# Performance work log

Hardware: AMD Instinct MI355X
Metric: run time of the kernel (lower is better)

Reference implementation:

```python
import jax, jax.numpy as jnp
import numpy as np

B, NEG = 2, 16            # queries, negatives per query
N, E, D = 10000, 80000, 128  # nodes, edges, feature dim (in_dim == out_dim)
NUM_REL = 237
L = 3                     # PNA layers
NODE_RATIO = 0.1
K = max(1, int(NODE_RATIO * N))  # static top-k: every repeated graph has exactly N nodes
EPS = 1e-5


def _score(hidden, rel, lin_W, lin_b, m1_W, m1_b, m2_W, m2_b):
    heur = jnp.concatenate([hidden, rel], axis=-1) @ lin_W + lin_b
    x = heur * hidden
    h = jax.nn.relu(x @ m1_W + m1_b)
    return jnp.squeeze(h @ m2_W + m2_b, -1)


def _pna_conv(hidden, src, dst, emask, deg, pre_W, pre_b, post_W, post_b, out_W, out_b):
    """PNA layer with mean/max/min/std aggregators and identity/amplification/attenuation
    scalers, restricted to edges where emask is True. deg is the (clamped >=1) degree used
    by the scalers."""
    BN = hidden.shape[0]
    # message: pre-linear on [x_i (target), x_j (source)] per edge  -> (Erep, D)
    m = jnp.concatenate([hidden[dst], hidden[src]], axis=-1) @ pre_W + pre_b
    w = emask.astype(hidden.dtype)[:, None]
    cnt = jax.ops.segment_sum(emask.astype(hidden.dtype), dst, num_segments=BN)
    denom = jnp.maximum(cnt, 1.0)[:, None]
    s1 = jax.ops.segment_sum(m * w, dst, num_segments=BN)
    s2 = jax.ops.segment_sum(m * m * w, dst, num_segments=BN)
    mean = s1 / denom
    var = jax.nn.relu(s2 / denom - mean * mean)
    std = jnp.sqrt(var + EPS)
    has = (cnt > 0)[:, None]
    mx = jnp.where(has, jax.ops.segment_max(jnp.where(emask[:, None], m, -jnp.inf), dst, num_segments=BN), 0.0)
    mn = jnp.where(has, jax.ops.segment_min(jnp.where(emask[:, None], m, jnp.inf), dst, num_segments=BN), 0.0)
    agg = jnp.concatenate([mean, mx, mn, std], axis=-1)           # (BN, 4D)
    logd = jnp.log(deg + 1.0)                                     # deg >= 1 -> logd > 0
    avg_log = jnp.mean(logd)
    agg = jnp.concatenate([agg, agg * (logd / avg_log)[:, None], agg * (avg_log / logd)[:, None]], axis=-1)  # (BN, 12D)
    return (agg @ post_W + post_b) @ out_W + out_b


def _forward(h_index, r_index, t_index, hidden_states, edge_index, rel_embedding,
             lin_W, lin_b, m1_W, m1_b, m2_W, m2_b, pre_W, pre_b, post_W, post_b, out_W, out_b):
    sc = (lin_W, lin_b, m1_W, m1_b, m2_W, m2_b)
    # negative_sample_to_tail
    is_t_neg = jnp.all(h_index == h_index[:, :1], axis=-1, keepdims=True)
    h_idx = jnp.where(is_t_neg, h_index, t_index)
    t_idx = jnp.where(is_t_neg, t_index, h_index)
    r_idx = jnp.where(is_t_neg, r_index, r_index + NUM_REL)
    # repeat_graph
    offsets = jnp.arange(B, dtype=h_idx.dtype) * N               # (B,)
    src = jnp.tile(edge_index[0], B) + jnp.repeat(offsets, E)    # (B*E,)
    dst = jnp.tile(edge_index[1], B) + jnp.repeat(offsets, E)
    BN = B * N
    rel_embeds = rel_embedding[r_idx[:, 0]].astype(hidden_states.dtype)  # (B, D)
    flat_h = h_idx[:, 0] + offsets
    flat_t = t_idx[:, 0] + offsets
    # literal `repeat_interleave(N, dim=0)[:B]` quirk -> row arange(B)//N of gathered embs
    sel = jnp.arange(B) // N
    h_vals = hidden_states[h_idx[:, 0]][sel]                     # (B, D)
    t_vals = hidden_states[t_idx[:, 0]][sel]
    # init_input_embeds: boundary condition + initial score at head nodes
    boundary = jnp.zeros((BN, D), hidden_states.dtype).at[flat_t].set(t_vals).at[flat_h].set(h_vals)
    score = jnp.zeros(BN, jnp.float32).at[flat_h].set(_score(h_vals, rel_embeds, *sc))
    hidden = boundary
    rel_per_node = jnp.repeat(rel_embeds, N, axis=0)             # (BN, D), rel_embeds[batch_rep]
    rows = jnp.arange(B)[:, None]
    for l in range(L):
        # select_edges_pyg with degree_ratio=1.0: all out-edges of per-graph top-k nodes
        _, idx = jax.lax.top_k(score.reshape(B, N), K)           # (B, K)
        node_sel = jnp.zeros((B, N), bool).at[rows, idx].set(True).reshape(-1)
        emask = node_sel[src]                                    # (B*E,) selected-edge mask
        out_deg = jax.ops.segment_sum(emask.astype(jnp.float32), src, num_segments=BN)
        deg_sub = jnp.maximum(out_deg.astype(hidden.dtype), 1.0)
        new_hidden = _pna_conv(hidden, src, dst, emask, deg_sub,
                               pre_W[l], pre_b[l], post_W[l], post_b[l], out_W[l], out_b[l])
        # residual only for nodes with selected outgoing edges
        hidden = jnp.where((out_deg > 0)[:, None], hidden + new_hidden, hidden)
        score = _score(hidden, rel_per_node, *sc)
    # read out scores at (repeated) tail indices -> (B, NEG)
    return score[t_idx + offsets[:, None]]


def setup_inputs() -> dict:
    key = jax.random.key(0)
    ks = jax.random.split(key, 14)
    s = 0.05
    hi = jax.random.randint(ks[0], (B, 1), 0, N)
    h_index = jnp.tile(hi, (1, NEG))                 # constant per row (assert in forward)
    r0 = jax.random.randint(ks[1], (B, 1), 0, NUM_REL)
    r_index = jnp.tile(r0, (1, NEG))                 # constant per row (assert in forward)
    t_index = jax.random.randint(ks[2], (B, NEG), 0, N)
    hidden_states = jax.random.normal(ks[3], (N, D), jnp.float32)
    edge_index = jax.random.randint(ks[4], (2, E), 0, N)
    return {
        "h_index": h_index, "r_index": r_index, "t_index": t_index,
        "hidden_states": hidden_states, "edge_index": edge_index,
        "rel_embedding": jax.random.normal(ks[5], (2 * NUM_REL, D), jnp.float32) * s,
        "lin_W": jax.random.normal(ks[6], (2 * D, D), jnp.float32) * s, "lin_b": jnp.zeros(D, jnp.float32),
        "m1_W": jax.random.normal(ks[7], (D, D), jnp.float32) * s, "m1_b": jnp.zeros(D, jnp.float32),
        "m2_W": jax.random.normal(ks[8], (D, 1), jnp.float32) * s, "m2_b": jnp.zeros(1, jnp.float32),
        "pre_W": jax.random.normal(ks[9], (L, 2 * D, D), jnp.float32) * s, "pre_b": jnp.zeros((L, D), jnp.float32),
        "post_W": jax.random.normal(ks[10], (L, 12 * D, D), jnp.float32) * s, "post_b": jnp.zeros((L, D), jnp.float32),
        "out_W": jax.random.normal(ks[11], (L, D, D), jnp.float32) * s, "out_b": jnp.zeros((L, D), jnp.float32),
    }


def reference(h_index, r_index, t_index, hidden_states, edge_index, rel_embedding,
              lin_W, lin_b, m1_W, m1_b, m2_W, m2_b, pre_W, pre_b, post_W, post_b, out_W, out_b):
    return _forward(h_index, r_index, t_index, hidden_states, edge_index, rel_embedding,
                    lin_W, lin_b, m1_W, m1_b, m2_W, m2_b, pre_W, pre_b, post_W, post_b, out_W, out_b)
```

## Files before the change

kernel.cpp:

```cpp
#include <hip/hip_runtime.h>
#include <math.h>

#define Bq 2
#define NEG 16
#define Nn 10000
#define Ee 80000
#define Dd 128
#define NUM_REL 237
#define Ll 3
#define K_SEL 1000
#define BN (Bq*Nn)
#define EPSV 1e-5f
#define MAXACT 2048
#define MAXTOUCH 8192
#define SELCAP 3328
#define LN2F 0.69314718056f

constexpr size_t HID_OFF   = 0;
constexpr size_t SCORE_OFF = HID_OFF   + (size_t)BN*Dd*4;
constexpr size_t CVEC_OFF  = SCORE_OFF + (size_t)BN*4;
constexpr size_t HDR_OFF   = CVEC_OFF  + (size_t)Bq*Dd*4;
constexpr size_t THR_OFF   = HDR_OFF   + 64*4;
constexpr size_t SEL_OFF   = THR_OFF   + Bq*8;
constexpr size_t DEG_OFF   = SEL_OFF   + (size_t)BN*4;
constexpr size_t SLOT_OFF  = DEG_OFF   + (size_t)BN*4;
constexpr size_t CNT_OFF   = SLOT_OFF  + (size_t)BN*4;
constexpr size_t SDEG_OFF  = CNT_OFF   + (size_t)MAXACT*4;
constexpr size_t S1_OFF    = SDEG_OFF  + (size_t)MAXACT*4;
constexpr size_t S2_OFF    = S1_OFF    + (size_t)MAXACT*Dd*4;
constexpr size_t MXB_OFF   = S2_OFF    + (size_t)MAXACT*Dd*4;
constexpr size_t MNB_OFF   = MXB_OFF   + (size_t)MAXACT*Dd*4;
constexpr size_t TPART_OFF = MNB_OFF   + (size_t)MAXACT*Dd*4;
constexpr size_t ALIST_OFF = TPART_OFF + (size_t)4*MAXACT*Dd*4;
constexpr size_t FLAG_OFF  = ALIST_OFF + (size_t)MAXACT*4;
constexpr size_t TLIST_OFF = FLAG_OFF  + (size_t)BN*4;
constexpr size_t EDGE_OFF  = TLIST_OFF + (size_t)MAXTOUCH*4;
constexpr size_t CTR_OFF   = EDGE_OFF  + (size_t)Bq*Ee*2*4;

__device__ __forceinline__ unsigned encf(float f){
  unsigned u = __float_as_uint(f);
  return (u & 0x80000000u) ? ~u : (u | 0x80000000u);
}
__device__ __forceinline__ float decf(unsigned e){
  unsigned u = (e & 0x80000000u) ? (e & 0x7FFFFFFFu) : ~e;
  return __uint_as_float(u);
}
__device__ __forceinline__ unsigned long long make_key(float f, int i){
  unsigned d = ~encf(f);
  return ((unsigned long long)d << 32) | (unsigned)i;
}

__global__ void k_zero(float* hidden, unsigned* flag){
  int i = blockIdx.x*blockDim.x + threadIdx.x;
  if (i < BN*Dd/4) ((float4*)hidden)[i] = make_float4(0.f,0.f,0.f,0.f);
  if (i < BN) flag[i] = 0u;
}

__global__ __launch_bounds__(256) void k_prep(
    const int* h_index, const int* r_index, const int* t_index,
    const float* hidden_states, const float* rel_embedding,
    const float* lin_W, const float* lin_b, const float* m1_W, const float* m1_b,
    const float* m2_W, const float* m2_b,
    int* hdr, float* cvec, float* hidden, float* score,
    unsigned* flag, int* tlist, unsigned* ctr){
  __shared__ int sh_fh[Bq], sh_ft[Bq], sh_r0[Bq], sh_hsrc, sh_tsrc;
  __shared__ float s_relv[Bq][Dd], s_cvec[Bq][Dd], s_hv[Dd], s_x[Bq][Dd], s_p[Bq][Dd];
  __shared__ float s_s0[Dd];
  __shared__ float sc0_sh;
  int tid = threadIdx.x;
  if (tid == 0){
    int n = 0;
    for (int b=0;b<Bq;b++){
      bool eq = true;
      for (int j=1;j<NEG;j++) eq = eq && (h_index[b*NEG+j]==h_index[b*NEG]);
      int h0 = eq ? h_index[b*NEG] : t_index[b*NEG];
      int t0 = eq ? t_index[b*NEG] : h_index[b*NEG];
      int r0 = eq ? r_index[b*NEG] : r_index[b*NEG] + NUM_REL;
      sh_fh[b] = h0 + b*Nn; sh_ft[b] = t0 + b*Nn; sh_r0[b] = r0;
      hdr[0+b] = sh_fh[b]; hdr[2+b] = sh_ft[b];
      for (int j=0;j<NEG;j++){
        int tj = eq ? t_index[b*NEG+j] : h_index[b*NEG+j];
        hdr[4 + b*NEG + j] = tj + b*Nn;
      }
      if (b==0){ sh_hsrc = h0; sh_tsrc = t0; }
      if (!flag[sh_ft[b]]){ flag[sh_ft[b]] = 1u; tlist[n++] = sh_ft[b]; }
      if (!flag[sh_fh[b]]){ flag[sh_fh[b]] = 1u; tlist[n++] = sh_fh[b]; }
    }
    ctr[3] = (unsigned)n;
  }
  __syncthreads();
  int b = tid >> 7, d = tid & 127;
  s_relv[b][d] = rel_embedding[(size_t)sh_r0[b]*Dd + d];
  if (b == 0){
    s_hv[d] = hidden_states[(size_t)sh_hsrc*Dd + d];
    s_s0[d] = fmaxf(m1_b[d], 0.f) * m2_W[d];
  }
  __syncthreads();
  if (tid == 0){
    float s = m2_b[0];
    for (int k=0;k<Dd;k++) s += s_s0[k];
    sc0_sh = s;
    ctr[4] = __float_as_uint(s);
  }
  float acc = lin_b[d];
  #pragma unroll 8
  for (int k=0;k<Dd;k++) acc += s_relv[b][k]*lin_W[(Dd+k)*Dd + d];
  s_cvec[b][d] = acc; cvec[b*Dd+d] = acc;
  hidden[(size_t)sh_ft[b]*Dd + d] = hidden_states[(size_t)sh_tsrc*Dd + d];
  hidden[(size_t)sh_fh[b]*Dd + d] = hidden_states[(size_t)sh_hsrc*Dd + d];
  __syncthreads();
  float sc0 = sc0_sh;
  for (int i = tid; i < BN; i += 256) score[i] = sc0;
  float hv = s_hv[d];
  float heur = s_cvec[b][d];
  #pragma unroll 8
  for (int k=0;k<Dd;k++) heur += s_hv[k]*lin_W[k*Dd + d];
  s_x[b][d] = heur * hv;
  __syncthreads();
  float a2 = m1_b[d];
  #pragma unroll 8
  for (int k=0;k<Dd;k++) a2 += s_x[b][k]*m1_W[k*Dd + d];
  s_p[b][d] = fmaxf(a2, 0.f) * m2_W[d];
  __syncthreads();
  if (tid < Bq){
    float s = m2_b[0];
    for (int k=0;k<Dd;k++) s += s_p[tid][k];
    score[sh_fh[tid]] = s;
  }
}

__global__ __launch_bounds__(256) void k_select(
    const float* score, const int* tlist, const unsigned* ctr,
    unsigned long long* thr){
  int b = blockIdx.x;
  int nt = (int)ctr[3];
  unsigned d0 = ~encf(__uint_as_float(ctr[4]));
  __shared__ unsigned sd[SELCAP];
  __shared__ unsigned short sidx[SELCAP];
  __shared__ unsigned hist[256], histT[256];
  __shared__ int ntb_sh;
  __shared__ unsigned long long pref_sh;
  __shared__ unsigned kk_sh;
  int tid = threadIdx.x;
  if (tid==0){ ntb_sh = 0; pref_sh = 0ull; kk_sh = K_SEL; }
  __syncthreads();
  int vlo = b*Nn, vhi = vlo + Nn;
  for (int i = tid; i < nt; i += 256){
    int v = tlist[i];
    if (v >= vlo && v < vhi){
      int pos = atomicAdd(&ntb_sh, 1);
      if (pos < SELCAP){
        sd[pos] = ~encf(score[v]);
        sidx[pos] = (unsigned short)(v - vlo);
      }
    }
  }
  __syncthreads();
  int ntb = min(ntb_sh, SELCAP);
  unsigned nvirt = (unsigned)(Nn - ntb);
  for (int pass = 7; pass >= 0; --pass){
    hist[tid] = 0u; histT[tid] = 0u;
    __syncthreads();
    unsigned long long pref = pref_sh;
    int sh_hi = 8*(pass+1);
    for (int j = tid; j < ntb; j += 256){
      unsigned long long key = ((unsigned long long)sd[j] << 32) | (unsigned long long)sidx[j];
      bool ok = (pass==7) || ((key >> sh_hi) == (pref >> sh_hi));
      if (ok) atomicAdd(&hist[(unsigned)(key >> (8*pass)) & 255u], 1u);
      if (pass < 4){
        unsigned idx = sidx[j];
        bool oki = (pass == 3) || ((idx >> sh_hi) == (((unsigned)pref) >> sh_hi));
        if (oki) atomicAdd(&histT[(idx >> (8*pass)) & 255u], 1u);
      }
    }
    __syncthreads();
    if (pass >= 4){
      if (tid == 0){
        unsigned long long keyv_hi = ((unsigned long long)d0 << 32);
        bool ok = (pass==7) || ((keyv_hi >> sh_hi) == (pref >> sh_hi));
        if (ok) atomicAdd(&hist[(d0 >> (8*(pass-4))) & 255u], nvirt);
      }
    } else {
      if ((unsigned)(pref >> 32) == d0){
        unsigned long long hf = 0ull;
        if (pass < 3) hf = (unsigned long long)((((unsigned)pref) >> sh_hi)) << sh_hi;
        unsigned long long lo = hf + ((unsigned long long)tid << (8*pass));
        unsigned long long hi = lo + (1ull << (8*pass));
        unsigned long long nn = (unsigned long long)Nn;
        unsigned long long l2 = lo < nn ? lo : nn;
        unsigned long long h2 = hi < nn ? hi : nn;
        if (h2 > l2){
          unsigned c = (unsigned)(h2 - l2) - histT[tid];
          if (c > 0u) atomicAdd(&hist[tid], c);
        }
      }
    }
    __syncthreads();
    if (tid < 256){
      unsigned kk = kk_sh;
      unsigned cum = 0;
      for (int i=0;i<tid;i++) cum += hist[i];
      unsigned h = hist[tid];
      if (h > 0u && cum < kk && kk <= cum + h){
        pref_sh |= ((unsigned long long)tid) << (8*pass);
        kk_sh = kk - cum;
      }
    }
    __syncthreads();
  }
  if (tid==0) thr[b] = pref_sh;
}

__global__ void k_mask(const float* score, const unsigned long long* thr, unsigned* sel,
                       unsigned* out_deg, float* s1, float* s2,
                       unsigned* mxb, unsigned* mnb, unsigned* cnt, unsigned* ctr){
  int i = blockIdx.x*blockDim.x + threadIdx.x;
  if (i < BN){
    int b = i / Nn; int v = i - b*Nn;
    sel[i] = (make_key(score[i], v) <= thr[b]) ? 1u : 0u;
    out_deg[i] = 0u;
  }
  if (i < MAXACT*Dd){ s1[i]=0.f; s2[i]=0.f; mxb[i]=0u; mnb[i]=0xFFFFFFFFu; }
  if (i < MAXACT) cnt[i]=0u;
  if (i < 3) ctr[i]=0u;
}

__global__ void k_degree(const int* ei, const unsigned* sel, unsigned* out_deg){
  int e = blockIdx.x*blockDim.x + threadIdx.x;
  if (e >= Ee) return;
  int s0 = ei[e];
  #pragma unroll
  for (int b=0;b<Bq;b++){
    int v = s0 + b*Nn;
    if (sel[v]) atomicAdd(&out_deg[v], 1u);
  }
}

__global__ void k_active(const unsigned* out_deg, int* node_slot, int* alist,
                         float* slot_deg, unsigned* ctr, unsigned* flag, int* tlist){
  int v = blockIdx.x*blockDim.x + threadIdx.x;
  if (v >= BN) return;
  unsigned dg = out_deg[v];
  if (dg > 0u){
    int slot = (int)atomicAdd(&ctr[0], 1u);
    alist[slot] = v; node_slot[v] = slot; slot_deg[slot] = (float)dg;
    atomicAdd((float*)&ctr[2], logf((float)dg + 1.0f));
    if (atomicExch(&flag[v], 1u) == 0u){
      int p = (int)atomicAdd(&ctr[3], 1u);
      tlist[p] = v;
    }
  }
}

__global__ void k_edges(const int* ei, const unsigned* sel, const unsigned* out_deg,
                        const int* node_slot, int* edges, unsigned* cnt, unsigned* ctr){
  int e = blockIdx.x*blockDim.x + threadIdx.x;
  if (e >= Ee) return;
  int s0 = ei[e], d0 = ei[Ee + e];
  #pragma unroll
  for (int b=0;b<Bq;b++){
    int s = s0 + b*Nn, dv = d0 + b*Nn;
    if (sel[s] && out_deg[dv] > 0u){
      int slot = node_slot[dv];
      int j = (int)atomicAdd(&ctr[1], 1u);
      edges[2*j] = s; edges[2*j+1] = slot;
      atomicAdd(&cnt[slot], 1u);
    }
  }
}

__global__ __launch_bounds__(128) void k_messages(
    const float* hidden, const int* edges, const int* alist,
    const float* preW, const float* preb,
    float* s1, float* s2, unsigned* mxb, unsigned* mnb, const unsigned* ctr){
  int ne = (int)ctr[1];
  int tid = threadIdx.x;
  __shared__ float sd[4][Dd], ss[4][Dd];
  __shared__ int dsl[4];
  float pb = preb[tid];
  for (int j0 = blockIdx.x*4; j0 < ne; j0 += gridDim.x*4){
    int nv = ne - j0; if (nv > 4) nv = 4;
    if (tid < 4){
      int j = j0 + ((tid < nv) ? tid : 0);
      dsl[tid] = edges[2*j+1];
    }
    #pragma unroll
    for (int e=0;e<4;e++){
      int j = j0 + ((e < nv) ? e : 0);
      int s = edges[2*j];
      int dv = alist[edges[2*j+1]];
      sd[e][tid] = hidden[(size_t)dv*Dd + tid];
      ss[e][tid] = hidden[(size_t)s*Dd + tid];
    }
    __syncthreads();
    float a[4] = {pb, pb, pb, pb};
    #pragma unroll 4
    for (int k=0;k<Dd;k++){
      float w0 = preW[k*Dd + tid];
      float w1 = preW[(Dd+k)*Dd + tid];
      #pragma unroll
      for (int e=0;e<4;e++) a[e] += sd[e][k]*w0 + ss[e][k]*w1;
    }
    for (int e=0;e<nv;e++){
      int dslot = dsl[e];
      atomicAdd(&s1[dslot*Dd + tid], a[e]);
      atomicAdd(&s2[dslot*Dd + tid], a[e]*a[e]);
      atomicMax(&mxb[dslot*Dd + tid], encf(a[e]));
      atomicMin(&mnb[dslot*Dd + tid], encf(a[e]));
    }
    __syncthreads();
  }
}

__global__ __launch_bounds__(512) void k_post(
    const unsigned* cnt, const float* s1, const float* s2,
    const unsigned* mxb, const unsigned* mnb, const float* slot_deg,
    const float* postW, float* tpart, const unsigned* ctr){
  int na = (int)ctr[0];
  int bid = blockIdx.x;
  int tile = bid & 63, ch = bid >> 6;
  if (tile*32 >= na) return;
  float logsum = __uint_as_float(ctr[2]);
  float avg = (logsum + (float)(BN - na)*LN2F) / (float)BN;
  __shared__ float lb[32*136];
  __shared__ float wbuf[3*16*128];
  __shared__ float sden[32];
  __shared__ unsigned shas[32];
  int tid = threadIdx.x;
  if (tid < 32){
    unsigned c = cnt[tile*32 + tid];
    sden[tid] = fmaxf((float)c, 1.0f);
    shas[tid] = c;
  }
  __syncthreads();
  for (int idx = tid; idx < 32*Dd; idx += 512){
    int sl = idx >> 7, kk = idx & 127;
    int gi = (tile*32 + sl)*Dd + kk;
    float den = sden[sl];
    float val;
    if (ch == 0)      val = s1[gi]/den;
    else if (ch == 1) val = shas[sl] ? decf(mxb[gi]) : 0.f;
    else if (ch == 2) val = shas[sl] ? decf(mnb[gi]) : 0.f;
    else {
      float mv = s1[gi]/den;
      float var = s2[gi]/den - mv*mv;
      val = sqrtf(fmaxf(var, 0.f) + EPSV);
    }
    lb[sl*136 + kk] = val;
  }
  int cg = tid & 31, rg = tid >> 5;
  int c0 = cg*4;
  float a0[2][4], a1[2][4], a2[2][4];
  #pragma unroll
  for (int i=0;i<2;i++)
    #pragma unroll
    for (int j=0;j<4;j++){ a0[i][j]=0.f; a1[i][j]=0.f; a2[i][j]=0.f; }
  for (int chunk = 0; chunk < 8; ++chunk){
    #pragma unroll
    for (int i = 0; i < 3; ++i){
      int f = tid + i*512;
      int q = f >> 9, r = f & 511;
      int kk = r >> 5, c4 = r & 31;
      int grow = q*512 + ch*128 + chunk*16 + kk;
      ((float4*)wbuf)[f] = *(const float4*)(postW + (size_t)grow*Dd + c4*4);
    }
    __syncthreads();
    #pragma unroll
    for (int k4 = 0; k4 < 4; ++k4){
      float4 av0 = *(const float4*)&lb[(rg*2+0)*136 + chunk*16 + k4*4];
      float4 av1 = *(const float4*)&lb[(rg*2+1)*136 + chunk*16 + k4*4];
      #pragma unroll
      for (int j = 0; j < 4; ++j){
        int kk = k4*4 + j;
        float4 w0 = *(const float4*)&wbuf[kk*128 + c0];
        float4 w1 = *(const float4*)&wbuf[(16+kk)*128 + c0];
        float4 w2 = *(const float4*)&wbuf[(32+kk)*128 + c0];
        float av[2] = { (&av0.x)[j], (&av1.x)[j] };
        #pragma unroll
        for (int i=0;i<2;i++){
          float a = av[i];
          a0[i][0] += a*w0.x; a0[i][1] += a*w0.y; a0[i][2] += a*w0.z; a0[i][3] += a*w0.w;
          a1[i][0] += a*w1.x; a1[i][1] += a*w1.y; a1[i][2] += a*w1.z; a1[i][3] += a*w1.w;
          a2[i][0] += a*w2.x; a2[i][1] += a*w2.y; a2[i][2] += a*w2.z; a2[i][3] += a*w2.w;
        }
      }
    }
    __syncthreads();
  }
  #pragma unroll
  for (int i=0;i<2;i++){
    int slot = tile*32 + rg*2 + i;
    if (slot < na){
      float dg = slot_deg[slot];
      float logd = logf(dg + 1.f);
      float al = logd/avg, be = avg/logd;
      float4 r;
      r.x = a0[i][0] + al*a1[i][0] + be*a2[i][0];
      r.y = a0[i][1] + al*a1[i][1] + be*a2[i][1];
      r.z = a0[i][2] + al*a1[i][2] + be*a2[i][2];
      r.w = a0[i][3] + al*a1[i][3] + be*a2[i][3];
      *(float4*)(tpart + (size_t)ch*MAXACT*Dd + (size_t)slot*Dd + c0) = r;
    }
  }
}

__global__ __launch_bounds__(256) void k_out_resid(
    const float* tpart, const int* alist, const float* outW, const float* outb,
    const float* postb, float* hidden, const unsigned* ctr){
  int na = (int)ctr[0];
  int tile = blockIdx.x;
  if (tile*32 >= na) return;
  __shared__ float tr[32*136];
  __shared__ float wbuf[16*128];
  int tid = threadIdx.x;
  for (int idx = tid; idx < 32*Dd; idx += 256){
    int sl = idx >> 7, kk = idx & 127;
    size_t o = (size_t)(tile*32 + sl)*Dd + kk;
    tr[sl*136 + kk] = tpart[o] + tpart[(size_t)MAXACT*Dd + o]
                    + tpart[(size_t)2*MAXACT*Dd + o] + tpart[(size_t)3*MAXACT*Dd + o]
                    + postb[kk];
  }
  int cg = tid & 31, rg = tid >> 5;
  int c0 = cg*4;
  float4 ob = *(const float4*)(outb + c0);
  float acc[4][4];
  #pragma unroll
  for (int r=0;r<4;r++){ acc[r][0]=ob.x; acc[r][1]=ob.y; acc[r][2]=ob.z; acc[r][3]=ob.w; }
  for (int chunk = 0; chunk < 8; ++chunk){
    #pragma unroll
    for (int i = 0; i < 2; ++i){
      int f = tid + i*256;
      int kk = f >> 5, c4 = f & 31;
      ((float4*)wbuf)[f] = *(const float4*)(outW + (size_t)(chunk*16 + kk)*Dd + c4*4);
    }
    __syncthreads();
    #pragma unroll
    for (int k4 = 0; k4 < 4; ++k4){
      float4 av[4];
      #pragma unroll
      for (int r=0;r<4;r++)
        av[r] = *(const float4*)&tr[(rg*4+r)*136 + chunk*16 + k4*4];
      #pragma unroll
      for (int j = 0; j < 4; ++j){
        float4 w = *(const float4*)&wbuf[(k4*4+j)*128 + c0];
        #pragma unroll
        for (int r=0;r<4;r++){
          float a = (&av[r].x)[j];
          acc[r][0] += a*w.x; acc[r][1] += a*w.y; acc[r][2] += a*w.z; acc[r][3] += a*w.w;
        }
      }
    }
    __syncthreads();
  }
  #pragma unroll
  for (int r=0;r<4;r++){
    int slot = tile*32 + rg*4 + r;
    if (slot < na){
      int v = alist[slot];
      float* hp = hidden + (size_t)v*Dd + c0;
      float4 h4 = *(float4*)hp;
      h4.x += acc[r][0]; h4.y += acc[r][1]; h4.z += acc[r][2]; h4.w += acc[r][3];
      *(float4*)hp = h4;
    }
  }
}

__global__ __launch_bounds__(256) void k_score(
    const float* hidden, const float* cvec, const float* linW,
    const float* m1W, const float* m1b, const float* m2W, const float* m2b,
    const int* tlist, const unsigned* ctr, float* score,
    const int* ovr, int ovr_n){
  int nt = (ovr_n > 0) ? ovr_n : (int)ctr[3];
  const int* list = (ovr_n > 0) ? ovr : tlist;
  int nb = blockIdx.x * 32;
  if (nb >= nt) return;
  __shared__ float sh[32*Dd];
  __shared__ float sx[32*Dd];
  __shared__ float sc[2*Dd];
  __shared__ int   sv[32];
  __shared__ float red[32*33];
  int tid = threadIdx.x;
  if (tid < 32){
    int idx = nb + tid;
    sv[tid] = (idx < nt) ? list[idx] : list[nb];
  }
  sc[tid] = cvec[tid];
  __syncthreads();
  for (int q = tid; q < 32*32; q += 256){
    int row = q >> 5, f4 = q & 31;
    ((float4*)sh)[row*32 + f4] = ((const float4*)(hidden + (size_t)sv[row]*Dd))[f4];
  }
  __syncthreads();
  int cg = tid & 31, rg = tid >> 5;
  int c0 = cg*4;
  float acc[4][4];
  #pragma unroll
  for (int i=0;i<4;i++){ acc[i][0]=0.f; acc[i][1]=0.f; acc[i][2]=0.f; acc[i][3]=0.f; }
  for (int k4=0;k4<32;k4++){
    float4 av[4];
    #pragma unroll
    for (int i=0;i<4;i++) av[i] = ((float4*)sh)[(rg*4+i)*32 + k4];
    #pragma unroll
    for (int j=0;j<4;j++){
      float4 w = *(const float4*)(linW + (size_t)(k4*4+j)*Dd + c0);
      #pragma unroll
      for (int i=0;i<4;i++){
        float a = (&av[i].x)[j];
        acc[i][0] += a*w.x; acc[i][1] += a*w.y; acc[i][2] += a*w.z; acc[i][3] += a*w.w;
      }
    }
  }
  #pragma unroll
  for (int i=0;i<4;i++){
    int row = rg*4 + i;
    int bb = (sv[row] >= Nn) ? 1 : 0;
    float4 cv = *(float4*)&sc[bb*Dd + c0];
    float4 hv = ((float4*)sh)[row*32 + cg];
    float4 x;
    x.x = (acc[i][0] + cv.x)*hv.x;
    x.y = (acc[i][1] + cv.y)*hv.y;
    x.z = (acc[i][2] + cv.z)*hv.z;
    x.w = (acc[i][3] + cv.w)*hv.w;
    ((float4*)sx)[row*32 + cg] = x;
  }
  __syncthreads();
  #pragma unroll
  for (int i=0;i<4;i++){ acc[i][0]=0.f; acc[i][1]=0.f; acc[i][2]=0.f; acc[i][3]=0.f; }
  for (int k4=0;k4<32;k4++){
    float4 av[4];
    #pragma unroll
    for (int i=0;i<4;i++) av[i] = ((float4*)sx)[(rg*4+i)*32 + k4];
    #pragma unroll
    for (int j=0;j<4;j++){
      float4 w = *(const float4*)(m1W + (size_t)(k4*4+j)*Dd + c0);
      #pragma unroll
      for (int i=0;i<4;i++){
        float a = (&av[i].x)[j];
        acc[i][0] += a*w.x; acc[i][1] += a*w.y; acc[i][2] += a*w.z; acc[i][3] += a*w.w;
      }
    }
  }
  float4 mb = *(const float4*)(m1b + c0);
  float4 mw = *(const float4*)(m2W + c0);
  #pragma unroll
  for (int i=0;i<4;i++){
    float p0 = fmaxf(acc[i][0]+mb.x, 0.f)*mw.x;
    float p1 = fmaxf(acc[i][1]+mb.y, 0.f)*mw.y;
    float p2 = fmaxf(acc[i][2]+mb.z, 0.f)*mw.z;
    float p3 = fmaxf(acc[i][3]+mb.w, 0.f)*mw.w;
    red[(rg*4+i)*33 + cg] = p0+p1+p2+p3;
  }
  __syncthreads();
  if (tid < 32){
    float s = m2b[0];
    for (int g=0; g<32; g++) s += red[tid*33 + g];
    if (nb + tid < nt) score[sv[tid]] = s;
  }
}

__global__ void k_gather(const float* score, const int* hdr, float* out){
  int i = threadIdx.x;
  if (i < Bq*NEG) out[i] = score[hdr[4+i]];
}

extern "C" void kernel_launch(void* const* d_in, const int* in_sizes, int n_in,
                              void* d_out, int out_size, void* d_ws, size_t ws_size,
                              hipStream_t stream){
  const int*   h_index       = (const int*)d_in[0];
  const int*   r_index       = (const int*)d_in[1];
  const int*   t_index       = (const int*)d_in[2];
  const float* hidden_states = (const float*)d_in[3];
  const int*   edge_index    = (const int*)d_in[4];
  const float* rel_embedding = (const float*)d_in[5];
  const float* lin_W  = (const float*)d_in[6];
  const float* lin_b  = (const float*)d_in[7];
  const float* m1_W   = (const float*)d_in[8];
  const float* m1_b   = (const float*)d_in[9];
  const float* m2_W   = (const float*)d_in[10];
  const float* m2_b   = (const float*)d_in[11];
  const float* pre_W  = (const float*)d_in[12];
  const float* pre_b  = (const float*)d_in[13];
  const float* post_W = (const float*)d_in[14];
  const float* post_b = (const float*)d_in[15];
  const float* out_W  = (const float*)d_in[16];
  const float* out_b  = (const float*)d_in[17];

  char* ws = (char*)d_ws;
  float*    hidden   = (float*)(ws + HID_OFF);
  float*    score    = (float*)(ws + SCORE_OFF);
  float*    cvec     = (float*)(ws + CVEC_OFF);
  int*      hdr      = (int*)(ws + HDR_OFF);
  unsigned long long* thr = (unsigned long long*)(ws + THR_OFF);
  unsigned* sel      = (unsigned*)(ws + SEL_OFF);
  unsigned* out_deg  = (unsigned*)(ws + DEG_OFF);
  int*      node_slot= (int*)(ws + SLOT_OFF);
  unsigned* cnt      = (unsigned*)(ws + CNT_OFF);
  float*    slot_deg = (float*)(ws + SDEG_OFF);
  float*    s1       = (float*)(ws + S1_OFF);
  float*    s2       = (float*)(ws + S2_OFF);
  unsigned* mxb      = (unsigned*)(ws + MXB_OFF);
  unsigned* mnb      = (unsigned*)(ws + MNB_OFF);
  float*    tpart    = (float*)(ws + TPART_OFF);
  int*      alist    = (int*)(ws + ALIST_OFF);
  unsigned* flag     = (unsigned*)(ws + FLAG_OFF);
  int*      tlist    = (int*)(ws + TLIST_OFF);
  int*      edges    = (int*)(ws + EDGE_OFF);
  unsigned* ctr      = (unsigned*)(ws + CTR_OFF);

  k_zero<<<(BN*Dd/4 + 255)/256, 256, 0, stream>>>(hidden, flag);
  k_prep<<<1, 256, 0, stream>>>(h_index, r_index, t_index, hidden_states, rel_embedding,
                                lin_W, lin_b, m1_W, m1_b, m2_W, m2_b,
                                hdr, cvec, hidden, score, flag, tlist, ctr);
  for (int l = 0; l < Ll; ++l){
    const float* preWl  = pre_W  + (size_t)l*2*Dd*Dd;
    const float* prebl  = pre_b  + (size_t)l*Dd;
    const float* postWl = post_W + (size_t)l*12*Dd*Dd;
    const float* postbl = post_b + (size_t)l*Dd;
    const float* outWl  = out_W  + (size_t)l*Dd*Dd;
    const float* outbl  = out_b  + (size_t)l*Dd;

    k_select<<<Bq, 256, 0, stream>>>(score, tlist, ctr, thr);
    k_mask<<<(MAXACT*Dd + 255)/256, 256, 0, stream>>>(score, thr, sel, out_deg,
                                                      s1, s2, mxb, mnb, cnt, ctr);
    k_degree<<<(Ee + 255)/256, 256, 0, stream>>>(edge_index, sel, out_deg);
    k_active<<<(BN + 255)/256, 256, 0, stream>>>(out_deg, node_slot, alist, slot_deg,
                                                 ctr, flag, tlist);
    k_edges<<<(Ee + 255)/256, 256, 0, stream>>>(edge_index, sel, out_deg, node_slot,
                                                edges, cnt, ctr);
    k_messages<<<512, 128, 0, stream>>>(hidden, edges, alist, preWl, prebl,
                                        s1, s2, mxb, mnb, ctr);
    k_post<<<256, 512, 0, stream>>>(cnt, s1, s2, mxb, mnb, slot_deg, postWl, tpart, ctr);
    k_out_resid<<<MAXACT/32, 256, 0, stream>>>(tpart, alist, outWl, outbl, postbl,
                                               hidden, ctr);
    if (l < Ll-1){
      k_score<<<MAXTOUCH/32, 256, 0, stream>>>(hidden, cvec, lin_W, m1_W, m1_b, m2_W, m2_b,
                                               tlist, ctr, score, tlist, 0);
    } else {
      k_score<<<1, 256, 0, stream>>>(hidden, cvec, lin_W, m1_W, m1_b, m2_W, m2_b,
                                     tlist, ctr, score, hdr + 4, Bq*NEG);
    }
  }
  k_gather<<<1, 64, 0, stream>>>(score, hdr, (float*)d_out);
}
```

Measured before the change: 481.7 us.

## Fuse init, selection/zeroing and edge-build kernels to cut launches per layer

Merges the zeroing and prep kernels into one multi-block init kernel. The top-k select now shares a launch with the workspace zeroing, and the selection mask is computed inline from score and threshold instead of being stored in a sel array. The active-node and edge-list kernels are combined into one build kernel, the message kernel is relaunched with a different grid and indexed by node slot, and the final score kernel writes the output directly so the gather kernel is gone. The aim is to remove several small kernel launches and passes over global memory in each of the three layers, at the cost of more complex combined kernels and recomputing the mask keys inside each edge kernel.

```diff
diff --git a/kernel.cpp b/kernel.cpp
--- a/kernel.cpp
+++ b/kernel.cpp
@@ -21,8 +21,8 @@
 constexpr size_t CVEC_OFF  = SCORE_OFF + (size_t)BN*4;
 constexpr size_t HDR_OFF   = CVEC_OFF  + (size_t)Bq*Dd*4;
 constexpr size_t THR_OFF   = HDR_OFF   + 64*4;
-constexpr size_t SEL_OFF   = THR_OFF   + Bq*8;
-constexpr size_t DEG_OFF   = SEL_OFF   + (size_t)BN*4;
+constexpr size_t INC_OFF   = THR_OFF   + Bq*8;
+constexpr size_t DEG_OFF   = INC_OFF   + (size_t)BN*4;
 constexpr size_t SLOT_OFF  = DEG_OFF   + (size_t)BN*4;
 constexpr size_t CNT_OFF   = SLOT_OFF  + (size_t)BN*4;
 constexpr size_t SDEG_OFF  = CNT_OFF   + (size_t)MAXACT*4;
@@ -50,272 +50,312 @@
   return ((unsigned long long)d << 32) | (unsigned)i;
 }
 
-__global__ void k_zero(float* hidden, unsigned* flag){
-  int i = blockIdx.x*blockDim.x + threadIdx.x;
-  if (i < BN*Dd/4) ((float4*)hidden)[i] = make_float4(0.f,0.f,0.f,0.f);
-  if (i < BN) flag[i] = 0u;
-}
-
-__global__ __launch_bounds__(256) void k_prep(
-    const int* h_index, const int* r_index, const int* t_index,
-    const float* hidden_states, const float* rel_embedding,
-    const float* lin_W, const float* lin_b, const float* m1_W, const float* m1_b,
-    const float* m2_W, const float* m2_b,
-    int* hdr, float* cvec, float* hidden, float* score,
-    unsigned* flag, int* tlist, unsigned* ctr){
-  __shared__ int sh_fh[Bq], sh_ft[Bq], sh_r0[Bq], sh_hsrc, sh_tsrc;
-  __shared__ float s_relv[Bq][Dd], s_cvec[Bq][Dd], s_hv[Dd], s_x[Bq][Dd], s_p[Bq][Dd];
-  __shared__ float s_s0[Dd];
-  __shared__ float sc0_sh;
-  int tid = threadIdx.x;
-  if (tid == 0){
-    int n = 0;
-    for (int b=0;b<Bq;b++){
-      bool eq = true;
-      for (int j=1;j<NEG;j++) eq = eq && (h_index[b*NEG+j]==h_index[b*NEG]);
-      int h0 = eq ? h_index[b*NEG] : t_index[b*NEG];
-      int t0 = eq ? t_index[b*NEG] : h_index[b*NEG];
-      int r0 = eq ? r_index[b*NEG] : r_index[b*NEG] + NUM_REL;
-      sh_fh[b] = h0 + b*Nn; sh_ft[b] = t0 + b*Nn; sh_r0[b] = r0;
-      hdr[0+b] = sh_fh[b]; hdr[2+b] = sh_ft[b];
-      for (int j=0;j<NEG;j++){
-        int tj = eq ? t_index[b*NEG+j] : h_index[b*NEG+j];
-        hdr[4 + b*NEG + j] = tj + b*Nn;
-      }
-      if (b==0){ sh_hsrc = h0; sh_tsrc = t0; }
-      if (!flag[sh_ft[b]]){ flag[sh_ft[b]] = 1u; tlist[n++] = sh_ft[b]; }
-      if (!flag[sh_fh[b]]){ flag[sh_fh[b]] = 1u; tlist[n++] = sh_fh[b]; }
-    }
-    ctr[3] = (unsigned)n;
-  }
-  __syncthreads();
-  int b = tid >> 7, d = tid & 127;
-  s_relv[b][d] = rel_embedding[(size_t)sh_r0[b]*Dd + d];
-  if (b == 0){
-    s_hv[d] = hidden_states[(size_t)sh_hsrc*Dd + d];
-    s_s0[d] = fmaxf(m1_b[d], 0.f) * m2_W[d];
-  }
+__global__ __launch_bounds__(256) void k_init(
+    const int* __restrict__ h_index, const int* __restrict__ r_index, const int* __restrict__ t_index,
+    const float* __restrict__ hidden_states, const float* __restrict__ rel_embedding,
+    const float* __restrict__ lin_W, const float* __restrict__ lin_b,
+    const float* __restrict__ m1_W, const float* __restrict__ m1_b,
+    const float* __restrict__ m2_W, const float* __restrict__ m2_b,
+    int* __restrict__ hdr, float* __restrict__ cvec, float* __restrict__ hidden,
+    float* __restrict__ score, unsigned* __restrict__ flag, int* __restrict__ tlist,
+    unsigned* __restrict__ ctr)
+{
+  __shared__ struct {
+    int hbuf[Bq*NEG], tbuf[Bq*NEG], rbuf[Bq*NEG];
+    int fh[Bq], ft[Bq], r0[Bq], eqf[Bq], hsrc, tsrc;
+    float s0red[Dd]; float sc0;
+    float relv[Bq][Dd], cv[Bq][Dd], hv[Dd], x[Bq][Dd], p[Bq][Dd];
+  } sp;
+  const int tid = threadIdx.x;
+  const int bid = blockIdx.x;
+  if (tid < Bq*NEG){
+    sp.hbuf[tid] = h_index[tid];
+    sp.tbuf[tid] = t_index[tid];
+    sp.rbuf[tid] = r_index[tid];
+  }
+  if (tid < Dd) sp.s0red[tid] = fmaxf(m1_b[tid], 0.f) * m2_W[tid];
   __syncthreads();
   if (tid == 0){
+    for (int b = 0; b < Bq; b++){
+      bool eq = true;
+      for (int j = 1; j < NEG; j++) eq = eq && (sp.hbuf[b*NEG+j] == sp.hbuf[b*NEG]);
+      int h0 = eq ? sp.hbuf[b*NEG] : sp.tbuf[b*NEG];
+      int t0 = eq ? sp.tbuf[b*NEG] : sp.hbuf[b*NEG];
+      int r0 = eq ? sp.rbuf[b*NEG] : sp.rbuf[b*NEG] + NUM_REL;
+      sp.fh[b] = h0 + b*Nn; sp.ft[b] = t0 + b*Nn;
+      sp.r0[b] = r0; sp.eqf[b] = eq ? 1 : 0;
+      if (b == 0){ sp.hsrc = h0; sp.tsrc = t0; }
+    }
     float s = m2_b[0];
-    for (int k=0;k<Dd;k++) s += s_s0[k];
-    sc0_sh = s;
-    ctr[4] = __float_as_uint(s);
-  }
-  float acc = lin_b[d];
-  #pragma unroll 8
-  for (int k=0;k<Dd;k++) acc += s_relv[b][k]*lin_W[(Dd+k)*Dd + d];
-  s_cvec[b][d] = acc; cvec[b*Dd+d] = acc;
-  hidden[(size_t)sh_ft[b]*Dd + d] = hidden_states[(size_t)sh_tsrc*Dd + d];
-  hidden[(size_t)sh_fh[b]*Dd + d] = hidden_states[(size_t)sh_hsrc*Dd + d];
+    for (int k = 0; k < Dd; k++) s += sp.s0red[k];
+    sp.sc0 = s;
+    if (bid == 0){
+      ctr[4] = __float_as_uint(s);
+      hdr[0] = sp.fh[0]; hdr[1] = sp.fh[1];
+      hdr[2] = sp.ft[0]; hdr[3] = sp.ft[1];
+      for (int b = 0; b < Bq; b++)
+        for (int j = 0; j < NEG; j++){
+          int tj = sp.eqf[b] ? sp.tbuf[b*NEG+j] : sp.hbuf[b*NEG+j];
+          hdr[4 + b*NEG + j] = tj + b*Nn;
+        }
+      int cand[4] = { sp.ft[0], sp.fh[0], sp.ft[1], sp.fh[1] };
+      int n = 0;
+      for (int c = 0; c < 4; c++){
+        bool dup = false;
+        for (int m = 0; m < n; m++) dup = dup || (tlist[m] == cand[c]);
+        if (!dup) tlist[n++] = cand[c];
+        flag[cand[c]] = 1u;
+      }
+      ctr[3] = (unsigned)n;
+    }
+  }
   __syncthreads();
-  float sc0 = sc0_sh;
-  for (int i = tid; i < BN; i += 256) score[i] = sc0;
-  float hv = s_hv[d];
-  float heur = s_cvec[b][d];
-  #pragma unroll 8
-  for (int k=0;k<Dd;k++) heur += s_hv[k]*lin_W[k*Dd + d];
-  s_x[b][d] = heur * hv;
-  __syncthreads();
-  float a2 = m1_b[d];
-  #pragma unroll 8
-  for (int k=0;k<Dd;k++) a2 += s_x[b][k]*m1_W[k*Dd + d];
-  s_p[b][d] = fmaxf(a2, 0.f) * m2_W[d];
-  __syncthreads();
-  if (tid < Bq){
-    float s = m2_b[0];
-    for (int k=0;k<Dd;k++) s += s_p[tid][k];
-    score[sh_fh[tid]] = s;
-  }
-}
-
-__global__ __launch_bounds__(256) void k_select(
-    const float* score, const int* tlist, const unsigned* ctr,
-    unsigned long long* thr){
-  int b = blockIdx.x;
-  int nt = (int)ctr[3];
-  unsigned d0 = ~encf(__uint_as_float(ctr[4]));
-  __shared__ unsigned sd[SELCAP];
-  __shared__ unsigned short sidx[SELCAP];
-  __shared__ unsigned hist[256], histT[256];
-  __shared__ int ntb_sh;
-  __shared__ unsigned long long pref_sh;
-  __shared__ unsigned kk_sh;
+  const int fh0 = sp.fh[0], fh1 = sp.fh[1];
+  const int ft0 = sp.ft[0], ft1 = sp.ft[1];
+  const float sc0 = sp.sc0;
+  if (bid == 0){
+    int b = tid >> 7, d = tid & 127;
+    sp.relv[b][d] = rel_embedding[(size_t)sp.r0[b]*Dd + d];
+    if (b == 0) sp.hv[d] = hidden_states[(size_t)sp.hsrc*Dd + d];
+    __syncthreads();
+    float acc = lin_b[d];
+    #pragma unroll 8
+    for (int k = 0; k < Dd; k++) acc += sp.relv[b][k]*lin_W[(Dd+k)*Dd + d];
+    sp.cv[b][d] = acc; cvec[b*Dd + d] = acc;
+    hidden[(size_t)sp.ft[b]*Dd + d] = hidden_states[(size_t)sp.tsrc*Dd + d];
+    hidden[(size_t)sp.fh[b]*Dd + d] = hidden_states[(size_t)sp.hsrc*Dd + d];
+    __syncthreads();
+    float hv = sp.hv[d];
+    float heur = sp.cv[b][d];
+    #pragma unroll 8
+    for (int k = 0; k < Dd; k++) heur += sp.hv[k]*lin_W[k*Dd + d];
+    sp.x[b][d] = heur * hv;
+    __syncthreads();
+    float a2 = m1_b[d];
+    #pragma unroll 8
+    for (int k = 0; k < Dd; k++) a2 += sp.x[b][k]*m1_W[k*Dd + d];
+    sp.p[b][d] = fmaxf(a2, 0.f) * m2_W[d];
+    __syncthreads();
+    if (tid < Bq){
+      float s = m2_b[0];
+      for (int k = 0; k < Dd; k++) s += sp.p[tid][k];
+      score[sp.fh[tid]] = s;
+    }
+  } else {
+    int zb = bid - 1, znb = gridDim.x - 1;
+    int zt = zb*256 + tid, zs = znb*256;
+    float4 z4 = make_float4(0.f, 0.f, 0.f, 0.f);
+    for (int i = zt; i < BN*32; i += zs){
+      int row = i >> 5;
+      if (row != ft0 && row != ft1 && row != fh0 && row != fh1)
+        ((float4*)hidden)[i] = z4;
+    }
+    for (int v = zt; v < BN; v += zs){
+      if (v != ft0 && v != ft1 && v != fh0 && v != fh1) flag[v] = 0u;
+      if (v != fh0 && v != fh1) score[v] = sc0;
+    }
+  }
+}
+
+__global__ __launch_bounds__(256) void k_selzero(
+    const float* __restrict__ score, const int* __restrict__ tlist,
+    unsigned long long* __restrict__ thr,
+    float* __restrict__ s1, float* __restrict__ s2,
+    unsigned* __restrict__ mxb, unsigned* __restrict__ mnb,
+    unsigned* __restrict__ out_deg, unsigned* __restrict__ incnt,
+    unsigned* __restrict__ ctr)
+{
   int tid = threadIdx.x;
-  if (tid==0){ ntb_sh = 0; pref_sh = 0ull; kk_sh = K_SEL; }
-  __syncthreads();
-  int vlo = b*Nn, vhi = vlo + Nn;
-  for (int i = tid; i < nt; i += 256){
-    int v = tlist[i];
-    if (v >= vlo && v < vhi){
-      int pos = atomicAdd(&ntb_sh, 1);
-      if (pos < SELCAP){
-        sd[pos] = ~encf(score[v]);
-        sidx[pos] = (unsigned short)(v - vlo);
-      }
-    }
-  }
-  __syncthreads();
-  int ntb = min(ntb_sh, SELCAP);
-  unsigned nvirt = (unsigned)(Nn - ntb);
-  for (int pass = 7; pass >= 0; --pass){
-    hist[tid] = 0u; histT[tid] = 0u;
-    __syncthreads();
-    unsigned long long pref = pref_sh;
-    int sh_hi = 8*(pass+1);
-    for (int j = tid; j < ntb; j += 256){
-      unsigned long long key = ((unsigned long long)sd[j] << 32) | (unsigned long long)sidx[j];
-      bool ok = (pass==7) || ((key >> sh_hi) == (pref >> sh_hi));
-      if (ok) atomicAdd(&hist[(unsigned)(key >> (8*pass)) & 255u], 1u);
-      if (pass < 4){
-        unsigned idx = sidx[j];
-        bool oki = (pass == 3) || ((idx >> sh_hi) == (((unsigned)pref) >> sh_hi));
-        if (oki) atomicAdd(&histT[(idx >> (8*pass)) & 255u], 1u);
-      }
-    }
-    __syncthreads();
-    if (pass >= 4){
-      if (tid == 0){
-        unsigned long long keyv_hi = ((unsigned long long)d0 << 32);
-        bool ok = (pass==7) || ((keyv_hi >> sh_hi) == (pref >> sh_hi));
-        if (ok) atomicAdd(&hist[(d0 >> (8*(pass-4))) & 255u], nvirt);
-      }
-    } else {
-      if ((unsigned)(pref >> 32) == d0){
-        unsigned long long hf = 0ull;
-        if (pass < 3) hf = (unsigned long long)((((unsigned)pref) >> sh_hi)) << sh_hi;
-        unsigned long long lo = hf + ((unsigned long long)tid << (8*pass));
-        unsigned long long hi = lo + (1ull << (8*pass));
-        unsigned long long nn = (unsigned long long)Nn;
-        unsigned long long l2 = lo < nn ? lo : nn;
-        unsigned long long h2 = hi < nn ? hi : nn;
-        if (h2 > l2){
-          unsigned c = (unsigned)(h2 - l2) - histT[tid];
-          if (c > 0u) atomicAdd(&hist[tid], c);
-        }
-      }
-    }
-    __syncthreads();
-    if (tid < 256){
-      unsigned kk = kk_sh;
-      unsigned cum = 0;
-      for (int i=0;i<tid;i++) cum += hist[i];
-      unsigned h = hist[tid];
-      if (h > 0u && cum < kk && kk <= cum + h){
-        pref_sh |= ((unsigned long long)tid) << (8*pass);
-        kk_sh = kk - cum;
-      }
-    }
-    __syncthreads();
-  }
-  if (tid==0) thr[b] = pref_sh;
-}
-
-__global__ void k_mask(const float* score, const unsigned long long* thr, unsigned* sel,
-                       unsigned* out_deg, float* s1, float* s2,
-                       unsigned* mxb, unsigned* mnb, unsigned* cnt, unsigned* ctr){
+  int bid = blockIdx.x;
+  if (bid < Bq){
+    int b = bid;
+    int nt = (int)ctr[3];
+    unsigned d0 = ~encf(__uint_as_float(ctr[4]));
+    __shared__ unsigned sd[SELCAP];
+    __shared__ unsigned short sidx[SELCAP];
+    __shared__ unsigned hist[256], histT[256];
+    __shared__ int ntb_sh;
+    __shared__ unsigned long long pref_sh;
+    __shared__ unsigned kk_sh;
+    if (tid == 0){ ntb_sh = 0; pref_sh = 0ull; kk_sh = K_SEL; }
+    __syncthreads();
+    int vlo = b*Nn, vhi = vlo + Nn;
+    for (int i = tid; i < nt; i += 256){
+      int v = tlist[i];
+      if (v >= vlo && v < vhi){
+        int pos = atomicAdd(&ntb_sh, 1);
+        if (pos < SELCAP){
+          sd[pos] = ~encf(score[v]);
+          sidx[pos] = (unsigned short)(v - vlo);
+        }
+      }
+    }
+    __syncthreads();
+    int ntb = min(ntb_sh, SELCAP);
+    unsigned nvirt = (unsigned)(Nn - ntb);
+    for (int pass = 7; pass >= 0; --pass){
+      hist[tid] = 0u; histT[tid] = 0u;
+      __syncthreads();
+      unsigned long long pref = pref_sh;
+      int sh_hi = 8*(pass+1);
+      for (int j = tid; j < ntb; j += 256){
+        unsigned long long key = ((unsigned long long)sd[j] << 32) | (unsigned long long)sidx[j];
+        bool ok = (pass==7) || ((key >> sh_hi) == (pref >> sh_hi));
+        if (ok) atomicAdd(&hist[(unsigned)(key >> (8*pass)) & 255u], 1u);
+        if (pass < 4){
+          unsigned idx = sidx[j];
+          bool oki = (pass == 3) || ((idx >> sh_hi) == (((unsigned)pref) >> sh_hi));
+          if (oki) atomicAdd(&histT[(idx >> (8*pass)) & 255u], 1u);
+        }
+      }
+      __syncthreads();
+      if (pass >= 4){
+        if (tid == 0){
+          unsigned long long keyv_hi = ((unsigned long long)d0 << 32);
+          bool ok = (pass==7) || ((keyv_hi >> sh_hi) == (pref_sh >> sh_hi));
+          if (ok) atomicAdd(&hist[(d0 >> (8*(pass-4))) & 255u], nvirt);
+        }
+      } else {
+        if ((unsigned)(pref >> 32) == d0){
+          unsigned long long hf = 0ull;
+          if (pass < 3) hf = (unsigned long long)((((unsigned)pref) >> sh_hi)) << sh_hi;
+          unsigned long long lo = hf + ((unsigned long long)tid << (8*pass));
+          unsigned long long hi = lo + (1ull << (8*pass));
+          unsigned long long nn = (unsigned long long)Nn;
+          unsigned long long l2 = lo < nn ? lo : nn;
+          unsigned long long h2 = hi < nn ? hi : nn;
+          if (h2 > l2){
+            unsigned c = (unsigned)(h2 - l2) - histT[tid];
+            if (c > 0u) atomicAdd(&hist[tid], c);
+          }
+        }
+      }
+      __syncthreads();
+      {
+        unsigned kk = kk_sh;
+        unsigned cum = 0;
+        for (int i = 0; i < tid; i++) cum += hist[i];
+        unsigned h = hist[tid];
+        if (h > 0u && cum < kk && kk <= cum + h){
+          pref_sh |= ((unsigned long long)tid) << (8*pass);
+          kk_sh = kk - cum;
+        }
+      }
+      __syncthreads();
+    }
+    if (tid == 0) thr[b] = pref_sh;
+  } else {
+    int zb = bid - Bq, znb = gridDim.x - Bq;
+    int zt = zb*256 + tid, zs = znb*256;
+    for (int i = zt; i < MAXACT*Dd; i += zs){
+      s1[i] = 0.f; s2[i] = 0.f; mxb[i] = 0u; mnb[i] = 0xFFFFFFFFu;
+    }
+    for (int i = zt; i < BN; i += zs){ out_deg[i] = 0u; incnt[i] = 0u; }
+    if (zt < 3) ctr[zt] = 0u;
+  }
+}
+
+__global__ void k_degree(const int* __restrict__ ei, const float* __restrict__ score,
+                         const unsigned long long* __restrict__ thr,
+                         unsigned* __restrict__ out_deg){
+  int e = blockIdx.x*blockDim.x + threadIdx.x;
+  if (e >= Ee) return;
+  unsigned long long th0 = thr[0], th1 = thr[1];
+  int s0 = ei[e];
+  if (make_key(score[s0], s0) <= th0) atomicAdd(&out_deg[s0], 1u);
+  int v1 = s0 + Nn;
+  if (make_key(score[v1], s0) <= th1) atomicAdd(&out_deg[v1], 1u);
+}
+
+__global__ void k_build(const int* __restrict__ ei, const float* __restrict__ score,
+                        const unsigned long long* __restrict__ thr,
+                        const unsigned* __restrict__ out_deg,
+                        int* __restrict__ node_slot, int* __restrict__ alist,
+                        float* __restrict__ slot_deg, unsigned* __restrict__ incnt,
+                        int* __restrict__ edges, unsigned* __restrict__ ctr,
+                        unsigned* __restrict__ flag, int* __restrict__ tlist){
   int i = blockIdx.x*blockDim.x + threadIdx.x;
   if (i < BN){
-    int b = i / Nn; int v = i - b*Nn;
-    sel[i] = (make_key(score[i], v) <= thr[b]) ? 1u : 0u;
-    out_deg[i] = 0u;
-  }
-  if (i < MAXACT*Dd){ s1[i]=0.f; s2[i]=0.f; mxb[i]=0u; mnb[i]=0xFFFFFFFFu; }
-  if (i < MAXACT) cnt[i]=0u;
-  if (i < 3) ctr[i]=0u;
-}
-
-__global__ void k_degree(const int* ei, const unsigned* sel, unsigned* out_deg){
-  int e = blockIdx.x*blockDim.x + threadIdx.x;
-  if (e >= Ee) return;
-  int s0 = ei[e];
-  #pragma unroll
-  for (int b=0;b<Bq;b++){
-    int v = s0 + b*Nn;
-    if (sel[v]) atomicAdd(&out_deg[v], 1u);
-  }
-}
-
-__global__ void k_active(const unsigned* out_deg, int* node_slot, int* alist,
-                         float* slot_deg, unsigned* ctr, unsigned* flag, int* tlist){
-  int v = blockIdx.x*blockDim.x + threadIdx.x;
-  if (v >= BN) return;
-  unsigned dg = out_deg[v];
-  if (dg > 0u){
-    int slot = (int)atomicAdd(&ctr[0], 1u);
-    alist[slot] = v; node_slot[v] = slot; slot_deg[slot] = (float)dg;
-    atomicAdd((float*)&ctr[2], logf((float)dg + 1.0f));
-    if (atomicExch(&flag[v], 1u) == 0u){
-      int p = (int)atomicAdd(&ctr[3], 1u);
-      tlist[p] = v;
-    }
-  }
-}
-
-__global__ void k_edges(const int* ei, const unsigned* sel, const unsigned* out_deg,
-                        const int* node_slot, int* edges, unsigned* cnt, unsigned* ctr){
-  int e = blockIdx.x*blockDim.x + threadIdx.x;
-  if (e >= Ee) return;
-  int s0 = ei[e], d0 = ei[Ee + e];
-  #pragma unroll
-  for (int b=0;b<Bq;b++){
-    int s = s0 + b*Nn, dv = d0 + b*Nn;
-    if (sel[s] && out_deg[dv] > 0u){
-      int slot = node_slot[dv];
+    unsigned dg = out_deg[i];
+    if (dg > 0u){
+      int slot = (int)atomicAdd(&ctr[0], 1u);
+      alist[slot] = i; node_slot[i] = slot; slot_deg[slot] = (float)dg;
+      atomicAdd((float*)&ctr[2], logf((float)dg + 1.0f));
+      if (atomicExch(&flag[i], 1u) == 0u){
+        int p = (int)atomicAdd(&ctr[3], 1u);
+        tlist[p] = i;
+      }
+    }
+  }
+  if (i < Ee){
+    unsigned long long th0 = thr[0], th1 = thr[1];
+    int s0 = ei[i], d0e = ei[Ee + i];
+    if (make_key(score[s0], s0) <= th0 && out_deg[d0e] > 0u){
       int j = (int)atomicAdd(&ctr[1], 1u);
-      edges[2*j] = s; edges[2*j+1] = slot;
-      atomicAdd(&cnt[slot], 1u);
-    }
-  }
-}
-
-__global__ __launch_bounds__(128) void k_messages(
-    const float* hidden, const int* edges, const int* alist,
-    const float* preW, const float* preb,
-    float* s1, float* s2, unsigned* mxb, unsigned* mnb, const unsigned* ctr){
+      edges[2*j] = s0; edges[2*j+1] = d0e;
+      atomicAdd(&incnt[d0e], 1u);
+    }
+    int sv = s0 + Nn, dv = d0e + Nn;
+    if (make_key(score[sv], s0) <= th1 && out_deg[dv] > 0u){
+      int j = (int)atomicAdd(&ctr[1], 1u);
+      edges[2*j] = sv; edges[2*j+1] = dv;
+      atomicAdd(&incnt[dv], 1u);
+    }
+  }
+}
+
+__global__ __launch_bounds__(256) void k_messages(
+    const float* __restrict__ hidden, const int* __restrict__ edges,
+    const int* __restrict__ node_slot,
+    const float* __restrict__ preW, const float* __restrict__ preb,
+    float* __restrict__ s1, float* __restrict__ s2,
+    unsigned* __restrict__ mxb, unsigned* __restrict__ mnb,
+    const unsigned* __restrict__ ctr){
   int ne = (int)ctr[1];
   int tid = threadIdx.x;
-  __shared__ float sd[4][Dd], ss[4][Dd];
-  __shared__ int dsl[4];
-  float pb = preb[tid];
-  for (int j0 = blockIdx.x*4; j0 < ne; j0 += gridDim.x*4){
-    int nv = ne - j0; if (nv > 4) nv = 4;
-    if (tid < 4){
-      int j = j0 + ((tid < nv) ? tid : 0);
-      dsl[tid] = edges[2*j+1];
-    }
-    #pragma unroll
-    for (int e=0;e<4;e++){
-      int j = j0 + ((e < nv) ? e : 0);
-      int s = edges[2*j];
-      int dv = alist[edges[2*j+1]];
-      sd[e][tid] = hidden[(size_t)dv*Dd + tid];
-      ss[e][tid] = hidden[(size_t)s*Dd + tid];
+  int half = tid >> 7, d = tid & 127;
+  __shared__ float sd[8][Dd], ss[8][Dd];
+  float pb = preb[d];
+  for (int j0 = blockIdx.x*8; j0 < ne; j0 += gridDim.x*8){
+    int base = j0 + half*4;
+    int nv = ne - base; if (nv > 4) nv = 4; if (nv < 0) nv = 0;
+    int dsl[4];
+    #pragma unroll
+    for (int e = 0; e < 4; e++){
+      int j = (e < nv) ? base + e : j0;
+      int s = edges[2*j]; int dv = edges[2*j+1];
+      dsl[e] = node_slot[dv];
+      sd[half*4+e][d] = hidden[(size_t)dv*Dd + d];
+      ss[half*4+e][d] = hidden[(size_t)s*Dd + d];
     }
     __syncthreads();
     float a[4] = {pb, pb, pb, pb};
     #pragma unroll 4
-    for (int k=0;k<Dd;k++){
-      float w0 = preW[k*Dd + tid];
-      float w1 = preW[(Dd+k)*Dd + tid];
+    for (int k = 0; k < Dd; k++){
+      float w0 = preW[k*Dd + d];
+      float w1 = preW[(Dd+k)*Dd + d];
       #pragma unroll
-      for (int e=0;e<4;e++) a[e] += sd[e][k]*w0 + ss[e][k]*w1;
-    }
-    for (int e=0;e<nv;e++){
+      for (int e = 0; e < 4; e++)
+        a[e] += sd[half*4+e][k]*w0 + ss[half*4+e][k]*w1;
+    }
+    for (int e = 0; e < nv; e++){
       int dslot = dsl[e];
-      atomicAdd(&s1[dslot*Dd + tid], a[e]);
-      atomicAdd(&s2[dslot*Dd + tid], a[e]*a[e]);
-      atomicMax(&mxb[dslot*Dd + tid], encf(a[e]));
-      atomicMin(&mnb[dslot*Dd + tid], encf(a[e]));
+      atomicAdd(&s1[dslot*Dd + d], a[e]);
+      atomicAdd(&s2[dslot*Dd + d], a[e]*a[e]);
+      atomicMax(&mxb[dslot*Dd + d], encf(a[e]));
+      atomicMin(&mnb[dslot*Dd + d], encf(a[e]));
     }
     __syncthreads();
   }
 }
 
 __global__ __launch_bounds__(512) void k_post(
-    const unsigned* cnt, const float* s1, const float* s2,
-    const unsigned* mxb, const unsigned* mnb, const float* slot_deg,
-    const float* postW, float* tpart, const unsigned* ctr){
+    const unsigned* __restrict__ incnt, const int* __restrict__ alist,
+    const float* __restrict__ s1, const float* __restrict__ s2,
+    const unsigned* __restrict__ mxb, const unsigned* __restrict__ mnb,
+    const float* __restrict__ slot_deg,
+    const float* __restrict__ postW, float* __restrict__ tpart,
+    const unsigned* __restrict__ ctr){
   int na = (int)ctr[0];
   int bid = blockIdx.x;
   int tile = bid & 63, ch = bid >> 6;
@@ -328,7 +368,8 @@
   __shared__ unsigned shas[32];
   int tid = threadIdx.x;
   if (tid < 32){
-    unsigned c = cnt[tile*32 + tid];
+    int slot = tile*32 + tid;
+    unsigned c = (slot < na) ? incnt[alist[slot]] : 0u;
     sden[tid] = fmaxf((float)c, 1.0f);
     shas[tid] = c;
   }
@@ -352,9 +393,9 @@
   int c0 = cg*4;
   float a0[2][4], a1[2][4], a2[2][4];
   #pragma unroll
-  for (int i=0;i<2;i++)
-    #pragma unroll
-    for (int j=0;j<4;j++){ a0[i][j]=0.f; a1[i][j]=0.f; a2[i][j]=0.f; }
+  for (int i = 0; i < 2; i++)
+    #pragma unroll
+    for (int j = 0; j < 4; j++){ a0[i][j]=0.f; a1[i][j]=0.f; a2[i][j]=0.f; }
   for (int chunk = 0; chunk < 8; ++chunk){
     #pragma unroll
     for (int i = 0; i < 3; ++i){
@@ -377,7 +418,7 @@
         float4 w2 = *(const float4*)&wbuf[(32+kk)*128 + c0];
         float av[2] = { (&av0.x)[j], (&av1.x)[j] };
         #pragma unroll
-        for (int i=0;i<2;i++){
+        for (int i = 0; i < 2; i++){
           float a = av[i];
           a0[i][0] += a*w0.x; a0[i][1] += a*w0.y; a0[i][2] += a*w0.z; a0[i][3] += a*w0.w;
           a1[i][0] += a*w1.x; a1[i][1] += a*w1.y; a1[i][2] += a*w1.z; a1[i][3] += a*w1.w;
@@ -388,7 +429,7 @@
     __syncthreads();
   }
   #pragma unroll
-  for (int i=0;i<2;i++){
+  for (int i = 0; i < 2; i++){
     int slot = tile*32 + rg*2 + i;
     if (slot < na){
       float dg = slot_deg[slot];
@@ -405,8 +446,10 @@
 }
 
 __global__ __launch_bounds__(256) void k_out_resid(
-    const float* tpart, const int* alist, const float* outW, const float* outb,
-    const float* postb, float* hidden, const unsigned* ctr){
+    const float* __restrict__ tpart, const int* __restrict__ alist,
+    const float* __restrict__ outW, const float* __restrict__ outb,
+    const float* __restrict__ postb, float* __restrict__ hidden,
+    const unsigned* __restrict__ ctr){
   int na = (int)ctr[0];
   int tile = blockIdx.x;
   if (tile*32 >= na) return;
@@ -425,7 +468,7 @@
   float4 ob = *(const float4*)(outb + c0);
   float acc[4][4];
   #pragma unroll
-  for (int r=0;r<4;r++){ acc[r][0]=ob.x; acc[r][1]=ob.y; acc[r][2]=ob.z; acc[r][3]=ob.w; }
+  for (int r = 0; r < 4; r++){ acc[r][0]=ob.x; acc[r][1]=ob.y; acc[r][2]=ob.z; acc[r][3]=ob.w; }
   for (int chunk = 0; chunk < 8; ++chunk){
     #pragma unroll
     for (int i = 0; i < 2; ++i){
@@ -438,13 +481,13 @@
     for (int k4 = 0; k4 < 4; ++k4){
       float4 av[4];
       #pragma unroll
-      for (int r=0;r<4;r++)
+      for (int r = 0; r < 4; r++)
         av[r] = *(const float4*)&tr[(rg*4+r)*136 + chunk*16 + k4*4];
       #pragma unroll
       for (int j = 0; j < 4; ++j){
         float4 w = *(const float4*)&wbuf[(k4*4+j)*128 + c0];
         #pragma unroll
-        for (int r=0;r<4;r++){
+        for (int r = 0; r < 4; r++){
           float a = (&av[r].x)[j];
           acc[r][0] += a*w.x; acc[r][1] += a*w.y; acc[r][2] += a*w.z; acc[r][3] += a*w.w;
         }
@@ -453,7 +496,7 @@
     __syncthreads();
   }
   #pragma unroll
-  for (int r=0;r<4;r++){
+  for (int r = 0; r < 4; r++){
     int slot = tile*32 + rg*4 + r;
     if (slot < na){
       int v = alist[slot];
@@ -466,10 +509,13 @@
 }
 
 __global__ __launch_bounds__(256) void k_score(
-    const float* hidden, const float* cvec, const float* linW,
-    const float* m1W, const float* m1b, const float* m2W, const float* m2b,
-    const int* tlist, const unsigned* ctr, float* score,
-    const int* ovr, int ovr_n){
+    const float* __restrict__ hidden, const float* __restrict__ cvec,
+    const float* __restrict__ linW,
+    const float* __restrict__ m1W, const float* __restrict__ m1b,
+    const float* __restrict__ m2W, const float* __restrict__ m2b,
+    const int* __restrict__ tlist, const unsigned* __restrict__ ctr,
+    float* __restrict__ score,
+    const int* __restrict__ ovr, int ovr_n, float* __restrict__ outp){
   int nt = (ovr_n > 0) ? ovr_n : (int)ctr[3];
   const int* list = (ovr_n > 0) ? ovr : tlist;
   int nb = blockIdx.x * 32;
@@ -495,23 +541,23 @@
   int c0 = cg*4;
   float acc[4][4];
   #pragma unroll
-  for (int i=0;i<4;i++){ acc[i][0]=0.f; acc[i][1]=0.f; acc[i][2]=0.f; acc[i][3]=0.f; }
-  for (int k4=0;k4<32;k4++){
+  for (int i = 0; i < 4; i++){ acc[i][0]=0.f; acc[i][1]=0.f; acc[i][2]=0.f; acc[i][3]=0.f; }
+  for (int k4 = 0; k4 < 32; k4++){
     float4 av[4];
     #pragma unroll
-    for (int i=0;i<4;i++) av[i] = ((float4*)sh)[(rg*4+i)*32 + k4];
-    #pragma unroll
-    for (int j=0;j<4;j++){
+    for (int i = 0; i < 4; i++) av[i] = ((float4*)sh)[(rg*4+i)*32 + k4];
+    #pragma unroll
+    for (int j = 0; j < 4; j++){
       float4 w = *(const float4*)(linW + (size_t)(k4*4+j)*Dd + c0);
       #pragma unroll
-      for (int i=0;i<4;i++){
+      for (int i = 0; i < 4; i++){
         float a = (&av[i].x)[j];
         acc[i][0] += a*w.x; acc[i][1] += a*w.y; acc[i][2] += a*w.z; acc[i][3] += a*w.w;
       }
     }
   }
   #pragma unroll
-  for (int i=0;i<4;i++){
+  for (int i = 0; i < 4; i++){
     int row = rg*4 + i;
     int bb = (sv[row] >= Nn) ? 1 : 0;
     float4 cv = *(float4*)&sc[bb*Dd + c0];
@@ -525,16 +571,16 @@
   }
   __syncthreads();
   #pragma unroll
-  for (int i=0;i<4;i++){ acc[i][0]=0.f; acc[i][1]=0.f; acc[i][2]=0.f; acc[i][3]=0.f; }
-  for (int k4=0;k4<32;k4++){
+  for (int i = 0; i < 4; i++){ acc[i][0]=0.f; acc[i][1]=0.f; acc[i][2]=0.f; acc[i][3]=0.f; }
+  for (int k4 = 0; k4 < 32; k4++){
     float4 av[4];
     #pragma unroll
-    for (int i=0;i<4;i++) av[i] = ((float4*)sx)[(rg*4+i)*32 + k4];
-    #pragma unroll
-    for (int j=0;j<4;j++){
+    for (int i = 0; i < 4; i++) av[i] = ((float4*)sx)[(rg*4+i)*32 + k4];
+    #pragma unroll
+    for (int j = 0; j < 4; j++){
       float4 w = *(const float4*)(m1W + (size_t)(k4*4+j)*Dd + c0);
       #pragma unroll
-      for (int i=0;i<4;i++){
+      for (int i = 0; i < 4; i++){
         float a = (&av[i].x)[j];
         acc[i][0] += a*w.x; acc[i][1] += a*w.y; acc[i][2] += a*w.z; acc[i][3] += a*w.w;
       }
@@ -543,7 +589,7 @@
   float4 mb = *(const float4*)(m1b + c0);
   float4 mw = *(const float4*)(m2W + c0);
   #pragma unroll
-  for (int i=0;i<4;i++){
+  for (int i = 0; i < 4; i++){
     float p0 = fmaxf(acc[i][0]+mb.x, 0.f)*mw.x;
     float p1 = fmaxf(acc[i][1]+mb.y, 0.f)*mw.y;
     float p2 = fmaxf(acc[i][2]+mb.z, 0.f)*mw.z;
@@ -553,14 +599,12 @@
   __syncthreads();
   if (tid < 32){
     float s = m2b[0];
-    for (int g=0; g<32; g++) s += red[tid*33 + g];
-    if (nb + tid < nt) score[sv[tid]] = s;
-  }
-}
-
-__global__ void k_gather(const float* score, const int* hdr, float* out){
-  int i = threadIdx.x;
-  if (i < Bq*NEG) out[i] = score[hdr[4+i]];
+    for (int g = 0; g < 32; g++) s += red[tid*33 + g];
+    if (nb + tid < nt){
+      if (ovr_n > 0) outp[nb + tid] = s;
+      else           score[sv[tid]] = s;
+    }
+  }
 }
 
 extern "C" void kernel_launch(void* const* d_in, const int* in_sizes, int n_in,
@@ -591,10 +635,9 @@
   float*    cvec     = (float*)(ws + CVEC_OFF);
   int*      hdr      = (int*)(ws + HDR_OFF);
   unsigned long long* thr = (unsigned long long*)(ws + THR_OFF);
-  unsigned* sel      = (unsigned*)(ws + SEL_OFF);
+  unsigned* incnt    = (unsigned*)(ws + INC_OFF);
   unsigned* out_deg  = (unsigned*)(ws + DEG_OFF);
   int*      node_slot= (int*)(ws + SLOT_OFF);
-  unsigned* cnt      = (unsigned*)(ws + CNT_OFF);
   float*    slot_deg = (float*)(ws + SDEG_OFF);
   float*    s1       = (float*)(ws + S1_OFF);
   float*    s2       = (float*)(ws + S2_OFF);
@@ -607,10 +650,9 @@
   int*      edges    = (int*)(ws + EDGE_OFF);
   unsigned* ctr      = (unsigned*)(ws + CTR_OFF);
 
-  k_zero<<<(BN*Dd/4 + 255)/256, 256, 0, stream>>>(hidden, flag);
-  k_prep<<<1, 256, 0, stream>>>(h_index, r_index, t_index, hidden_states, rel_embedding,
-                                lin_W, lin_b, m1_W, m1_b, m2_W, m2_b,
-                                hdr, cvec, hidden, score, flag, tlist, ctr);
+  k_init<<<416, 256, 0, stream>>>(h_index, r_index, t_index, hidden_states, rel_embedding,
+                                  lin_W, lin_b, m1_W, m1_b, m2_W, m2_b,
+                                  hdr, cvec, hidden, score, flag, tlist, ctr);
   for (int l = 0; l < Ll; ++l){
     const float* preWl  = pre_W  + (size_t)l*2*Dd*Dd;
     const float* prebl  = pre_b  + (size_t)l*Dd;
@@ -619,26 +661,24 @@
     const float* outWl  = out_W  + (size_t)l*Dd*Dd;
     const float* outbl  = out_b  + (size_t)l*Dd;
 
-    k_select<<<Bq, 256, 0, stream>>>(score, tlist, ctr, thr);
-    k_mask<<<(MAXACT*Dd + 255)/256, 256, 0, stream>>>(score, thr, sel, out_deg,
-                                                      s1, s2, mxb, mnb, cnt, ctr);
-    k_degree<<<(Ee + 255)/256, 256, 0, stream>>>(edge_index, sel, out_deg);
-    k_active<<<(BN + 255)/256, 256, 0, stream>>>(out_deg, node_slot, alist, slot_deg,
-                                                 ctr, flag, tlist);
-    k_edges<<<(Ee + 255)/256, 256, 0, stream>>>(edge_index, sel, out_deg, node_slot,
-                                                edges, cnt, ctr);
-    k_messages<<<512, 128, 0, stream>>>(hidden, edges, alist, preWl, prebl,
+    k_selzero<<<130, 256, 0, stream>>>(score, tlist, thr, s1, s2, mxb, mnb,
+                                       out_deg, incnt, ctr);
+    k_degree<<<(Ee + 255)/256, 256, 0, stream>>>(edge_index, score, thr, out_deg);
+    k_build<<<(Ee + 255)/256, 256, 0, stream>>>(edge_index, score, thr, out_deg,
+                                                node_slot, alist, slot_deg, incnt,
+                                                edges, ctr, flag, tlist);
+    k_messages<<<384, 256, 0, stream>>>(hidden, edges, node_slot, preWl, prebl,
                                         s1, s2, mxb, mnb, ctr);
-    k_post<<<256, 512, 0, stream>>>(cnt, s1, s2, mxb, mnb, slot_deg, postWl, tpart, ctr);
+    k_post<<<256, 512, 0, stream>>>(incnt, alist, s1, s2, mxb, mnb, slot_deg,
+                                    postWl, tpart, ctr);
     k_out_resid<<<MAXACT/32, 256, 0, stream>>>(tpart, alist, outWl, outbl, postbl,
                                                hidden, ctr);
     if (l < Ll-1){
       k_score<<<MAXTOUCH/32, 256, 0, stream>>>(hidden, cvec, lin_W, m1_W, m1_b, m2_W, m2_b,
-                                               tlist, ctr, score, tlist, 0);
+                                               tlist, ctr, score, tlist, 0, score);
     } else {
       k_score<<<1, 256, 0, stream>>>(hidden, cvec, lin_W, m1_W, m1_b, m2_W, m2_b,
-                                     tlist, ctr, score, hdr + 4, Bq*NEG);
-    }
-  }
-  k_gather<<<1, 64, 0, stream>>>(score, hdr, (float*)d_out);
-}
+                                     tlist, ctr, score, hdr + 4, Bq*NEG, (float*)d_out);
+    }
+  }
+}
```

Result: faster. 443.3 us (-8.0%).
